# Kernel tuning notes

Hardware: AMD Instinct MI355X
Metric: run time of the kernel (lower is better)

## Reference

```python
import jax, jax.numpy as jnp
import numpy as np

IMG = 448; P = 16; C = 3; D = 512; DC = 8; DS = 4
NH = IMG // P            # 28 patches per side
NPATCH = NH * NH         # 784
PDIM = C * P * P         # 768
BATCH = 32
EPS = 1e-5


def setup_inputs() -> dict:
    key = jax.random.key(0)
    ks = jax.random.split(key, 10)
    def lin(k, fan_in, shape):
        bound = 1.0 / np.sqrt(fan_in)
        return jax.random.uniform(k, shape, jnp.float32, -bound, bound)
    return {
        "images": jax.random.normal(ks[0], (BATCH, C, IMG, IMG), jnp.float32),
        "W_patch": lin(ks[1], PDIM, (PDIM, D)),
        "b_patch": jnp.zeros((D,), jnp.float32),
        "pos_embed": jax.random.normal(ks[2], (1, NPATCH, D), jnp.float32) * 0.02,
        "W_coord": lin(ks[3], D, (D, DC)),
        "b_coord": jnp.zeros((DC,), jnp.float32),
        "W_spinor": lin(ks[4], D, (D, DS)),
        "b_spinor": jnp.zeros((DS,), jnp.float32),
        "W_embed": lin(ks[5], DC, (DC, D)),
        "b_embed": jnp.zeros((D,), jnp.float32),
        "ln_gamma": jnp.ones((D,), jnp.float32),
        "ln_beta": jnp.zeros((D,), jnp.float32),
        "W_out": lin(ks[6], D, (D, D)),
        "b_out": jnp.zeros((D,), jnp.float32),
    }


def reference(images, W_patch, b_patch, pos_embed, W_coord, b_coord,
              W_spinor, b_spinor, W_embed, b_embed,
              ln_gamma, ln_beta, W_out, b_out):
    B = images.shape[0]
    # patchify == F.unfold(kernel=stride=P).transpose(1,2):
    # patches[b, bh*NH+bw, c*P*P + i*P + j] = images[b, c, bh*P+i, bw*P+j]
    patches = images.reshape(B, C, NH, P, NH, P)
    patches = patches.transpose(0, 2, 4, 1, 3, 5).reshape(B, NPATCH, PDIM)
    # patch embed + positional embedding  -> (B, NPATCH, D)
    x = patches @ W_patch + b_patch + pos_embed
    # manifold projection: coords (B,N,DC), spinor (B,N,DS)
    coords = x @ W_coord + b_coord
    spinor = x @ W_spinor + b_spinor
    # K0 scalar bilinear: psi^T psi -> (B, N)
    K0 = jnp.sum(spinor * spinor, axis=-1)
    # embed back from manifold coords -> (B, N, D)
    x_manifold = coords @ W_embed + b_embed
    # K0-modulated remix + residual
    x_enh = x_manifold * K0[..., None] + x
    # output projection: LayerNorm -> Linear
    mu = jnp.mean(x_enh, axis=-1, keepdims=True)
    var = jnp.mean(jnp.square(x_enh - mu), axis=-1, keepdims=True)
    x_norm = (x_enh - mu) * jax.lax.rsqrt(var + EPS) * ln_gamma + ln_beta
    return x_norm @ W_out + b_out
```

## Files before the change

kernel.cpp:

```cpp
#include <hip/hip_runtime.h>
#include <hip/hip_bf16.h>
#include <stdint.h>


typedef __bf16 bf16_t;
typedef bf16_t bf16x8 __attribute__((ext_vector_type(8)));
typedef bf16_t bf16x4 __attribute__((ext_vector_type(4)));
typedef float  f32x4  __attribute__((ext_vector_type(4)));

#define IMG     448
#define PSZ     16
#define NHP     28
#define NPATCH  784
#define PDIM    768
#define DMODEL  512
#define MROWS   25088

__device__ __forceinline__ void gload16(void* lds, const void* g) {
  __builtin_amdgcn_global_load_lds(
      (__attribute__((address_space(1))) void*)(uintptr_t)g,
      (__attribute__((address_space(3))) void*)lds,
      16, 0, 0);
}

__device__ __forceinline__ unsigned short bfbits(float v) {
  bf16_t h = (bf16_t)v;
  unsigned short u;
  __builtin_memcpy(&u, &h, 2);
  return u;
}
__device__ __forceinline__ float f_from_bits(unsigned u) {
  float f; __builtin_memcpy(&f, &u, 4); return f;
}

__global__ __launch_bounds__(256) void transpose_to_bf16(
    const float* __restrict__ src, bf16_t* __restrict__ dst, int K, int N)
{
  __shared__ float t[64][65];
  const int tx = threadIdx.x;
  const int ty = threadIdx.y;
  const int bx = blockIdx.x * 64;
  const int by = blockIdx.y * 64;
  #pragma unroll
  for (int r = ty; r < 64; r += 4)
    t[r][tx] = src[(size_t)(by + r) * N + (bx + tx)];
  __syncthreads();
  #pragma unroll
  for (int r = ty; r < 64; r += 4)
    dst[(size_t)(bx + r) * K + (by + tx)] = (bf16_t)t[tx][r];
}

__global__ __launch_bounds__(256) void manifold_prep(
    const float* __restrict__ Wc, const float* __restrict__ Ws,
    const float* __restrict__ We, const float* __restrict__ be,
    bf16_t* __restrict__ Wcsg, bf16_t* __restrict__ We2g)
{
  const int idx = blockIdx.x * 256 + threadIdx.x;
  if (idx < 8192) {
    const int r = idx >> 9, n = idx & 511;
    float v = 0.f;
    if (r < 8)       v = Wc[n * 8 + r];
    else if (r < 12) v = Ws[n * 4 + (r - 8)];
    Wcsg[idx] = (bf16_t)v;
  } else {
    const int j = idx - 8192;
    const int n = j >> 4, k = j & 15;
    float v = 0.f;
    if (k < 8)       v = We[k * 512 + n];
    else if (k == 8) v = be[n];
    We2g[j] = (bf16_t)v;
  }
}

__global__ __launch_bounds__(256) void patchify_bf16(
    const float* __restrict__ images, bf16_t* __restrict__ Apat)
{
  __shared__ bf16_t t[16][456];
  const int tid = threadIdx.x;
  const int bid = blockIdx.x;
  const int b = bid / 84, rem = bid % 84;
  const int c = rem / 28, ph = rem % 28;
  const float* src = images + ((size_t)(b * 3 + c) * IMG + ph * PSZ) * IMG;

  #pragma unroll
  for (int idx = tid; idx < 16 * 112; idx += 256) {
    const int i = idx / 112, x4 = idx % 112;
    const float4 v = *(const float4*)(src + (size_t)i * IMG + x4 * 4);
    bf16x4 w;
    w[0] = (bf16_t)v.x; w[1] = (bf16_t)v.y; w[2] = (bf16_t)v.z; w[3] = (bf16_t)v.w;
    *(bf16x4*)&t[i][x4 * 4] = w;
  }
  __syncthreads();

  const size_t mbase = (size_t)b * NPATCH + (size_t)ph * NHP;
  #pragma unroll
  for (int idx = tid; idx < 28 * 64; idx += 256) {
    const int pw = idx >> 6, e = idx & 63;
    const int i = e >> 2, j4 = e & 3;
    const bf16x4 w = *(const bf16x4*)&t[i][pw * 16 + j4 * 4];
    *(bf16x4*)&Apat[(mbase + pw) * PDIM + c * 256 + i * 16 + j4 * 4] = w;
  }
}

template<int KDIM, int EPI>
__global__ __launch_bounds__(256) void gemm_bf16(
    const bf16_t* __restrict__ A, const bf16_t* __restrict__ BT,
    const float* __restrict__ bias, const float* __restrict__ pos,
    void* __restrict__ outp)
{
  __shared__ bf16_t As[64 * 64];
  __shared__ bf16_t Bs[128 * 64];
  constexpr int NT = KDIM / 64;

  const int tid  = threadIdx.x;
  const int orig = blockIdx.x;
  const int wg   = (orig & 7) * 196 + (orig >> 3);
  const int n0   = (wg & 3) * 128;
  const int m0   = (wg >> 2) * 64;

  const int wave = tid >> 6, lane = tid & 63;

  const int ra = lane >> 3;
  const int ca = (lane & 7) ^ ra;
  const bf16_t* ag = A  + (size_t)(m0 + wave * 8 + ra) * KDIM + ca * 8;
  const bf16_t* bg = BT + (size_t)(n0 + wave * 8 + ra) * KDIM + ca * 8;
  bf16_t* al0 = As + (wave * 8) * 64;
  bf16_t* al1 = As + (wave * 8 + 32) * 64;
  bf16_t* bl0 = Bs + (wave * 8) * 64;
  bf16_t* bl1 = Bs + (wave * 8 + 32) * 64;
  bf16_t* bl2 = Bs + (wave * 8 + 64) * 64;
  bf16_t* bl3 = Bs + (wave * 8 + 96) * 64;

  const int wm = (wave >> 1) * 32;
  const int wn = (wave & 1) * 64;
  const int lr = lane & 15;
  const int lt = lane >> 4;

  f32x4 acc[2][4] = {};

  for (int t = 0; t < NT; ++t) {
    const int k0 = t * 64;
    __syncthreads();
    gload16(al0, ag + k0);
    gload16(al1, ag + 32 * KDIM + k0);
    gload16(bl0, bg + k0);
    gload16(bl1, bg + 32 * KDIM + k0);
    gload16(bl2, bg + 64 * KDIM + k0);
    gload16(bl3, bg + 96 * KDIM + k0);
    __syncthreads();

    #pragma unroll
    for (int ks = 0; ks < 2; ++ks) {
      const int c = ks * 4 + lt;
      bf16x8 af[2], bfr[4];
      #pragma unroll
      for (int i = 0; i < 2; ++i) {
        const int row = wm + i * 16 + lr;
        af[i] = *(const bf16x8*)&As[row * 64 + ((c ^ (row & 7)) * 8)];
      }
      #pragma unroll
      for (int j = 0; j < 4; ++j) {
        const int row = wn + j * 16 + lr;
        bfr[j] = *(const bf16x8*)&Bs[row * 64 + ((c ^ (row & 7)) * 8)];
      }
      #pragma unroll
      for (int i = 0; i < 2; ++i)
        #pragma unroll
        for (int j = 0; j < 4; ++j)
          acc[i][j] = __builtin_amdgcn_mfma_f32_16x16x32_bf16(af[i], bfr[j], acc[i][j], 0, 0, 0);
    }
  }

  const int q4 = lt << 2;
  const int colb = n0 + wn;
  #pragma unroll
  for (int i = 0; i < 2; ++i) {
    #pragma unroll
    for (int r = 0; r < 4; ++r) {
      const int mm = m0 + wm + i * 16 + q4 + r;
      if (EPI == 0) {
        const int pp = mm % NPATCH;
        const float* pe = pos + (size_t)pp * DMODEL;
        bf16_t* orow = (bf16_t*)outp + (size_t)mm * DMODEL;
        #pragma unroll
        for (int j = 0; j < 4; ++j) {
          const int nn = colb + j * 16 + lr;
          orow[nn] = (bf16_t)(acc[i][j][r] + bias[nn] + pe[nn]);
        }
      } else {
        float* orow = (float*)outp + (size_t)mm * DMODEL;
        #pragma unroll
        for (int j = 0; j < 4; ++j) {
          const int nn = colb + j * 16 + lr;
          orow[nn] = acc[i][j][r] + bias[nn];
        }
      }
    }
  }
}

__global__ __launch_bounds__(256) void gemm1_fused_fallback(
    const float* __restrict__ images, const bf16_t* __restrict__ WpT,
    const float* __restrict__ b_patch, const float* __restrict__ pos_embed,
    bf16_t* __restrict__ xout)
{
  __shared__ bf16_t As[128][40];
  __shared__ bf16_t Bs[128][40];
  const int tid = threadIdx.x;
  const int n0 = blockIdx.x * 128;
  const int m0 = blockIdx.y * 128;
  const int sr = tid >> 1;
  const int sh = tid & 1;
  const int m  = m0 + sr;
  const int b  = m / NPATCH;
  const int p  = m - b * NPATCH;
  const int ph = p / NHP;
  const int pw = p - ph * NHP;
  const float* abase = images + (size_t)(b * 3) * (IMG * IMG)
                              + (size_t)(ph * PSZ) * IMG + pw * PSZ;
  const bf16_t* brow = WpT + (size_t)(n0 + sr) * PDIM + sh * 16;
  const int wave = tid >> 6;
  const int lane = tid & 63;
  const int wm = (wave >> 1) << 6;
  const int wn = (wave & 1) << 6;
  const int lr = lane & 15;
  const int lk = (lane >> 4) << 3;
  f32x4 acc[4][4] = {};
  for (int ks = 0; ks < PDIM / 32; ++ks) {
    const int k0 = ks * 32;
    const int c  = k0 >> 8;
    const int ib = (k0 >> 4) & 15;
    const float* asrc = abase + (size_t)c * (IMG * IMG) + (ib + sh) * IMG;
    const float4 av0 = *(const float4*)(asrc + 0);
    const float4 av1 = *(const float4*)(asrc + 4);
    const float4 av2 = *(const float4*)(asrc + 8);
    const float4 av3 = *(const float4*)(asrc + 12);
    const uint4 bv0 = *(const uint4*)(brow + k0);
    const uint4 bv1 = *(const uint4*)(brow + k0 + 8);
    __syncthreads();
    bf16x8 a0, a1;
    a0[0] = (bf16_t)av0.x; a0[1] = (bf16_t)av0.y; a0[2] = (bf16_t)av0.z; a0[3] = (bf16_t)av0.w;
    a0[4] = (bf16_t)av1.x; a0[5] = (bf16_t)av1.y; a0[6] = (bf16_t)av1.z; a0[7] = (bf16_t)av1.w;
    a1[0] = (bf16_t)av2.x; a1[1] = (bf16_t)av2.y; a1[2] = (bf16_t)av2.z; a1[3] = (bf16_t)av2.w;
    a1[4] = (bf16_t)av3.x; a1[5] = (bf16_t)av3.y; a1[6] = (bf16_t)av3.z; a1[7] = (bf16_t)av3.w;
    *(bf16x8*)&As[sr][sh * 16]     = a0;
    *(bf16x8*)&As[sr][sh * 16 + 8] = a1;
    *(uint4*)&Bs[sr][sh * 16]      = bv0;
    *(uint4*)&Bs[sr][sh * 16 + 8]  = bv1;
    __syncthreads();
    bf16x8 af[4], bfr[4];
    #pragma unroll
    for (int i = 0; i < 4; ++i) af[i]  = *(const bf16x8*)&As[wm + i * 16 + lr][lk];
    #pragma unroll
    for (int j = 0; j < 4; ++j) bfr[j] = *(const bf16x8*)&Bs[wn + j * 16 + lr][lk];
    #pragma unroll
    for (int i = 0; i < 4; ++i)
      #pragma unroll
      for (int j = 0; j < 4; ++j)
        acc[i][j] = __builtin_amdgcn_mfma_f32_16x16x32_bf16(af[i], bfr[j], acc[i][j], 0, 0, 0);
  }
  const int colb = n0 + wn;
  #pragma unroll
  for (int i = 0; i < 4; ++i) {
    #pragma unroll
    for (int r = 0; r < 4; ++r) {
      const int mm = m0 + wm + i * 16 + ((lane >> 4) << 2) + r;
      const int pp = mm % NPATCH;
      const float* pe = pos_embed + (size_t)pp * DMODEL;
      bf16_t* orow = xout + (size_t)mm * DMODEL;
      #pragma unroll
      for (int j = 0; j < 4; ++j) {
        const int nn = colb + j * 16 + lr;
        orow[nn] = (bf16_t)(acc[i][j][r] + b_patch[nn] + pe[nn]);
      }
    }
  }
}

__global__ __launch_bounds__(256) void manifold_ln_v4(
    bf16_t* __restrict__ x,
    const bf16_t* __restrict__ Wcsg, const bf16_t* __restrict__ We2g,
    const float* __restrict__ b_coord, const float* __restrict__ b_spinor,
    const float* __restrict__ ln_gamma, const float* __restrict__ ln_beta)
{
  __shared__ bf16_t sWcs[16 * 512];
  __shared__ bf16_t sWe2[512 * 16];
  __shared__ float  sg[512], sb[512];

  const int tid = threadIdx.x;

  #pragma unroll
  for (int i = 0; i < 4; ++i) {
    const int c = tid + 256 * i;
    const int r = c >> 6, off = (c & 63) * 16;
    const uint4 v = *(const uint4*)((const char*)Wcsg + (size_t)c * 16);
    *(uint4*)((char*)sWcs + ((r * 1024 + off) ^ ((r & 7) << 4))) = v;
  }
  #pragma unroll
  for (int i = 0; i < 4; ++i) {
    const int c = tid + 256 * i;
    const int n = c >> 1, half = (c & 1) * 16;
    const uint4 v = *(const uint4*)((const char*)We2g + (size_t)c * 16);
    *(uint4*)((char*)sWe2 + ((n * 32 + half) ^ ((n & 3) << 4))) = v;
  }
  for (int i = tid; i < 512; i += 256) {
    sg[i] = ln_gamma[i];
    sb[i] = ln_beta[i];
  }
  __syncthreads();

  const int w    = tid >> 6;
  const int lane = tid & 63;
  const int lr   = lane & 15;
  const int lk   = (lane >> 4) << 3;
  const int q4   = (lane >> 4) << 2;
  const int m0w  = blockIdx.x * 64 + w * 16;

  float bbv[4];
  #pragma unroll
  for (int r = 0; r < 4; ++r) {
    if (q4 == 0)      bbv[r] = b_coord[r];
    else if (q4 == 4) bbv[r] = b_coord[4 + r];
    else if (q4 == 8) bbv[r] = b_spinor[r];
    else              bbv[r] = 0.f;
  }

  const bf16_t* xrow = x + (size_t)(m0w + lr) * DMODEL + lk;
  f32x4 acc1 = {0.f, 0.f, 0.f, 0.f};
  #pragma unroll
  for (int ks = 0; ks < 16; ++ks) {
    const bf16x8 bf = *(const bf16x8*)(xrow + ks * 32);
    const int wb = (lr * 1024 + ks * 64 + lk * 2) ^ ((lr & 7) << 4);
    const bf16x8 wf = *(const bf16x8*)((const char*)sWcs + wb);
    acc1 = __builtin_amdgcn_mfma_f32_16x16x32_bf16(wf, bf, acc1, 0, 0, 0);
  }

  float sv[4];
  #pragma unroll
  for (int r = 0; r < 4; ++r) sv[r] = acc1[r] + bbv[r];

  const float k0own = sv[0] * sv[0] + sv[1] * sv[1] + sv[2] * sv[2] + sv[3] * sv[3];
  const float k0v = __shfl(k0own, 32 + lr, 64);

  float ov[4];
  #pragma unroll
  for (int r = 0; r < 4; ++r) ov[r] = __shfl_xor(sv[r], 16, 64);

  const bf16_t zb = (bf16_t)0.f;
  bf16x8 b2;
  if (lk == 0) {
    #pragma unroll
    for (int r = 0; r < 4; ++r) { b2[r] = (bf16_t)sv[r]; b2[4 + r] = (bf16_t)ov[r]; }
  } else if (lk == 8) {
    b2[0] = (bf16_t)1.0f;
    #pragma unroll
    for (int t = 1; t < 8; ++t) b2[t] = zb;
  } else {
    #pragma unroll
    for (int t = 0; t < 8; ++t) b2[t] = zb;
  }

  const bf16_t* xres = x + (size_t)(m0w + lr) * DMODEL + q4;
  unsigned xpA[32], xpB[32];
  float s1 = 0.f, s2 = 0.f;
  #pragma unroll
  for (int nf = 0; nf < 32; ++nf) {
    const int n = nf * 16 + lr;
    const int wb = (n * 32 + lk * 2) ^ ((n & 3) << 4);
    const bf16x8 wf = *(const bf16x8*)((const char*)sWe2 + wb);
    f32x4 acc2 = {0.f, 0.f, 0.f, 0.f};
    acc2 = __builtin_amdgcn_mfma_f32_16x16x32_bf16(wf, b2, acc2, 0, 0, 0);

    const bf16x4 xr = *(const bf16x4*)(xres + nf * 16);
    float xe[4];
    #pragma unroll
    for (int r = 0; r < 4; ++r) {
      xe[r] = acc2[r] * k0v + (float)xr[r];
      s1 += xe[r];
      s2 += xe[r] * xe[r];
    }
    xpA[nf] = (unsigned)bfbits(xe[0]) | ((unsigned)bfbits(xe[1]) << 16);
    xpB[nf] = (unsigned)bfbits(xe[2]) | ((unsigned)bfbits(xe[3]) << 16);
  }

  s1 += __shfl_xor(s1, 16, 64);
  s1 += __shfl_xor(s1, 32, 64);
  s2 += __shfl_xor(s2, 16, 64);
  s2 += __shfl_xor(s2, 32, 64);
  const float mu  = s1 * (1.f / 512.f);
  const float var = s2 * (1.f / 512.f) - mu * mu;
  const float rsg = rsqrtf(var + 1e-5f);

  bf16_t* xo = x + (size_t)(m0w + lr) * DMODEL + q4;
  #pragma unroll
  for (int nf = 0; nf < 32; ++nf) {
    const f32x4 g = *(const f32x4*)&sg[nf * 16 + q4];
    const f32x4 b = *(const f32x4*)&sb[nf * 16 + q4];
    const float v0 = f_from_bits(xpA[nf] << 16);
    const float v1 = f_from_bits(xpA[nf] & 0xffff0000u);
    const float v2 = f_from_bits(xpB[nf] << 16);
    const float v3 = f_from_bits(xpB[nf] & 0xffff0000u);
    bf16x4 o;
    o[0] = (bf16_t)((v0 - mu) * rsg * g[0] + b[0]);
    o[1] = (bf16_t)((v1 - mu) * rsg * g[1] + b[1]);
    o[2] = (bf16_t)((v2 - mu) * rsg * g[2] + b[2]);
    o[3] = (bf16_t)((v3 - mu) * rsg * g[3] + b[3]);
    *(bf16x4*)(xo + nf * 16) = o;
  }
}

extern "C" void kernel_launch(void* const* d_in, const int* in_sizes, int n_in,
                              void* d_out, int out_size, void* d_ws, size_t ws_size,
                              hipStream_t stream)
{
  const float* images    = (const float*)d_in[0];
  const float* W_patch   = (const float*)d_in[1];
  const float* b_patch   = (const float*)d_in[2];
  const float* pos_embed = (const float*)d_in[3];
  const float* W_coord   = (const float*)d_in[4];
  const float* b_coord   = (const float*)d_in[5];
  const float* W_spinor  = (const float*)d_in[6];
  const float* b_spinor  = (const float*)d_in[7];
  const float* W_embed   = (const float*)d_in[8];
  const float* b_embed   = (const float*)d_in[9];
  const float* ln_gamma  = (const float*)d_in[10];
  const float* ln_beta   = (const float*)d_in[11];
  const float* W_out     = (const float*)d_in[12];
  const float* b_out     = (const float*)d_in[13];
  float* out = (float*)d_out;

  const size_t SZ_APAT = (size_t)MROWS * PDIM * 2;
  const size_t SZ_X    = (size_t)MROWS * DMODEL * 2;
  const size_t SZ_WPT  = (size_t)DMODEL * PDIM * 2;
  const size_t SZ_WOT  = (size_t)DMODEL * DMODEL * 2;
  const size_t SZ_WCS  = 16 * 512 * 2;
  const size_t SZ_WE2  = 512 * 16 * 2;
  const size_t NEED_FULL = SZ_APAT + SZ_X + SZ_WPT + SZ_WOT + SZ_WCS + SZ_WE2;

  char* ws = (char*)d_ws;
  const bool full = (ws_size >= NEED_FULL);

  bf16_t *Apat, *x, *WpT, *WoT, *Wcsg, *We2g;
  if (full) {
    char* p = ws;
    Apat  = (bf16_t*)p;            p += SZ_APAT;
    x     = (bf16_t*)p;            p += SZ_X;
    WpT   = (bf16_t*)p;            p += SZ_WPT;
    WoT   = (bf16_t*)p;            p += SZ_WOT;
    Wcsg  = (bf16_t*)p;            p += SZ_WCS;
    We2g  = (bf16_t*)p;
  } else {
    char* p = ws;
    Apat  = nullptr;
    x     = (bf16_t*)p;            p += SZ_X;
    WpT   = (bf16_t*)p;            p += SZ_WPT;
    WoT   = (bf16_t*)p;            p += SZ_WOT;
    Wcsg  = (bf16_t*)p;            p += SZ_WCS;
    We2g  = (bf16_t*)p;
  }

  hipLaunchKernelGGL(transpose_to_bf16, dim3(8, 12), dim3(64, 4), 0, stream,
                     W_patch, WpT, PDIM, DMODEL);
  hipLaunchKernelGGL(transpose_to_bf16, dim3(8, 8), dim3(64, 4), 0, stream,
                     W_out, WoT, DMODEL, DMODEL);
  hipLaunchKernelGGL(manifold_prep, dim3(64), dim3(256), 0, stream,
                     W_coord, W_spinor, W_embed, b_embed, Wcsg, We2g);

  if (full) {
    hipLaunchKernelGGL(patchify_bf16, dim3(32 * 3 * 28), dim3(256), 0, stream,
                       images, Apat);
    hipLaunchKernelGGL((gemm_bf16<PDIM, 0>), dim3(1568), dim3(256), 0, stream,
                       Apat, WpT, b_patch, pos_embed, (void*)x);
  } else {
    hipLaunchKernelGGL(gemm1_fused_fallback, dim3(4, 196), dim3(256), 0, stream,
                       images, WpT, b_patch, pos_embed, x);
  }

  hipLaunchKernelGGL(manifold_ln_v4, dim3(392), dim3(256), 0, stream,
                     x, Wcsg, We2g, b_coord, b_spinor, ln_gamma, ln_beta);

  hipLaunchKernelGGL((gemm_bf16<DMODEL, 1>), dim3(1568), dim3(256), 0, stream,
                     x, WoT, b_out, (const float*)nullptr, (void*)out);
}
```

Before: 114.5 us.

## Split manifold+LayerNorm into coords/K0 kernel and row-wise embed+LN kernel

Replaces the single fused manifold_ln kernel with two kernels. coords_k0 computes the coords and K0 per row with an MFMA and stores them in a small fp32 buffer. embed_ln then rebuilds x_manifold with scalar FMAs from register-resident W_embed and applies LayerNorm, one row per wave with fully coalesced 16-byte accesses. The intent is to drop the LDS staging, the second tiny MFMA and the 64 packed registers per thread, for better occupancy and memory access. In exchange x is read twice plus one extra launch and a small buffer round trip, and x_manifold and b_embed now stay in fp32 instead of bf16.

```diff
diff --git a/kernel.cpp b/kernel.cpp
--- a/kernel.cpp
+++ b/kernel.cpp
@@ -23,16 +23,6 @@
       16, 0, 0);
 }
 
-__device__ __forceinline__ unsigned short bfbits(float v) {
-  bf16_t h = (bf16_t)v;
-  unsigned short u;
-  __builtin_memcpy(&u, &h, 2);
-  return u;
-}
-__device__ __forceinline__ float f_from_bits(unsigned u) {
-  float f; __builtin_memcpy(&f, &u, 4); return f;
-}
-
 __global__ __launch_bounds__(256) void transpose_to_bf16(
     const float* __restrict__ src, bf16_t* __restrict__ dst, int K, int N)
 {
@@ -52,8 +42,7 @@
 
 __global__ __launch_bounds__(256) void manifold_prep(
     const float* __restrict__ Wc, const float* __restrict__ Ws,
-    const float* __restrict__ We, const float* __restrict__ be,
-    bf16_t* __restrict__ Wcsg, bf16_t* __restrict__ We2g)
+    bf16_t* __restrict__ Wcsg)
 {
   const int idx = blockIdx.x * 256 + threadIdx.x;
   if (idx < 8192) {
@@ -62,13 +51,6 @@
     if (r < 8)       v = Wc[n * 8 + r];
     else if (r < 12) v = Ws[n * 4 + (r - 8)];
     Wcsg[idx] = (bf16_t)v;
-  } else {
-    const int j = idx - 8192;
-    const int n = j >> 4, k = j & 15;
-    float v = 0.f;
-    if (k < 8)       v = We[k * 512 + n];
-    else if (k == 8) v = be[n];
-    We2g[j] = (bf16_t)v;
   }
 }
 
@@ -277,44 +259,16 @@
   }
 }
 
-__global__ __launch_bounds__(256) void manifold_ln_v4(
-    bf16_t* __restrict__ x,
-    const bf16_t* __restrict__ Wcsg, const bf16_t* __restrict__ We2g,
+__global__ __launch_bounds__(64) void coords_k0(
+    const bf16_t* __restrict__ x, const bf16_t* __restrict__ Wcsg,
     const float* __restrict__ b_coord, const float* __restrict__ b_spinor,
-    const float* __restrict__ ln_gamma, const float* __restrict__ ln_beta)
-{
-  __shared__ bf16_t sWcs[16 * 512];
-  __shared__ bf16_t sWe2[512 * 16];
-  __shared__ float  sg[512], sb[512];
-
-  const int tid = threadIdx.x;
-
-  #pragma unroll
-  for (int i = 0; i < 4; ++i) {
-    const int c = tid + 256 * i;
-    const int r = c >> 6, off = (c & 63) * 16;
-    const uint4 v = *(const uint4*)((const char*)Wcsg + (size_t)c * 16);
-    *(uint4*)((char*)sWcs + ((r * 1024 + off) ^ ((r & 7) << 4))) = v;
-  }
-  #pragma unroll
-  for (int i = 0; i < 4; ++i) {
-    const int c = tid + 256 * i;
-    const int n = c >> 1, half = (c & 1) * 16;
-    const uint4 v = *(const uint4*)((const char*)We2g + (size_t)c * 16);
-    *(uint4*)((char*)sWe2 + ((n * 32 + half) ^ ((n & 3) << 4))) = v;
-  }
-  for (int i = tid; i < 512; i += 256) {
-    sg[i] = ln_gamma[i];
-    sb[i] = ln_beta[i];
-  }
-  __syncthreads();
-
-  const int w    = tid >> 6;
-  const int lane = tid & 63;
+    float* __restrict__ Cbuf)
+{
+  const int lane = threadIdx.x;
   const int lr   = lane & 15;
   const int lk   = (lane >> 4) << 3;
   const int q4   = (lane >> 4) << 2;
-  const int m0w  = blockIdx.x * 64 + w * 16;
+  const int m0w  = blockIdx.x * 16;
 
   float bbv[4];
   #pragma unroll
@@ -326,12 +280,12 @@
   }
 
   const bf16_t* xrow = x + (size_t)(m0w + lr) * DMODEL + lk;
+  const bf16_t* wrow = Wcsg + lr * DMODEL + lk;
   f32x4 acc1 = {0.f, 0.f, 0.f, 0.f};
   #pragma unroll
   for (int ks = 0; ks < 16; ++ks) {
     const bf16x8 bf = *(const bf16x8*)(xrow + ks * 32);
-    const int wb = (lr * 1024 + ks * 64 + lk * 2) ^ ((lr & 7) << 4);
-    const bf16x8 wf = *(const bf16x8*)((const char*)sWcs + wb);
+    const bf16x8 wf = *(const bf16x8*)(wrow + ks * 32);
     acc1 = __builtin_amdgcn_mfma_f32_16x16x32_bf16(wf, bf, acc1, 0, 0, 0);
   }
 
@@ -339,73 +293,86 @@
   #pragma unroll
   for (int r = 0; r < 4; ++r) sv[r] = acc1[r] + bbv[r];
 
-  const float k0own = sv[0] * sv[0] + sv[1] * sv[1] + sv[2] * sv[2] + sv[3] * sv[3];
-  const float k0v = __shfl(k0own, 32 + lr, 64);
-
-  float ov[4];
-  #pragma unroll
-  for (int r = 0; r < 4; ++r) ov[r] = __shfl_xor(sv[r], 16, 64);
-
-  const bf16_t zb = (bf16_t)0.f;
-  bf16x8 b2;
-  if (lk == 0) {
-    #pragma unroll
-    for (int r = 0; r < 4; ++r) { b2[r] = (bf16_t)sv[r]; b2[4 + r] = (bf16_t)ov[r]; }
-  } else if (lk == 8) {
-    b2[0] = (bf16_t)1.0f;
-    #pragma unroll
-    for (int t = 1; t < 8; ++t) b2[t] = zb;
-  } else {
-    #pragma unroll
-    for (int t = 0; t < 8; ++t) b2[t] = zb;
-  }
-
-  const bf16_t* xres = x + (size_t)(m0w + lr) * DMODEL + q4;
-  unsigned xpA[32], xpB[32];
-  float s1 = 0.f, s2 = 0.f;
-  #pragma unroll
-  for (int nf = 0; nf < 32; ++nf) {
-    const int n = nf * 16 + lr;
-    const int wb = (n * 32 + lk * 2) ^ ((n & 3) << 4);
-    const bf16x8 wf = *(const bf16x8*)((const char*)sWe2 + wb);
-    f32x4 acc2 = {0.f, 0.f, 0.f, 0.f};
-    acc2 = __builtin_amdgcn_mfma_f32_16x16x32_bf16(wf, b2, acc2, 0, 0, 0);
-
-    const bf16x4 xr = *(const bf16x4*)(xres + nf * 16);
-    float xe[4];
-    #pragma unroll
-    for (int r = 0; r < 4; ++r) {
-      xe[r] = acc2[r] * k0v + (float)xr[r];
-      s1 += xe[r];
-      s2 += xe[r] * xe[r];
-    }
-    xpA[nf] = (unsigned)bfbits(xe[0]) | ((unsigned)bfbits(xe[1]) << 16);
-    xpB[nf] = (unsigned)bfbits(xe[2]) | ((unsigned)bfbits(xe[3]) << 16);
-  }
-
-  s1 += __shfl_xor(s1, 16, 64);
-  s1 += __shfl_xor(s1, 32, 64);
-  s2 += __shfl_xor(s2, 16, 64);
-  s2 += __shfl_xor(s2, 32, 64);
-  const float mu  = s1 * (1.f / 512.f);
-  const float var = s2 * (1.f / 512.f) - mu * mu;
-  const float rsg = rsqrtf(var + 1e-5f);
-
-  bf16_t* xo = x + (size_t)(m0w + lr) * DMODEL + q4;
-  #pragma unroll
-  for (int nf = 0; nf < 32; ++nf) {
-    const f32x4 g = *(const f32x4*)&sg[nf * 16 + q4];
-    const f32x4 b = *(const f32x4*)&sb[nf * 16 + q4];
-    const float v0 = f_from_bits(xpA[nf] << 16);
-    const float v1 = f_from_bits(xpA[nf] & 0xffff0000u);
-    const float v2 = f_from_bits(xpB[nf] << 16);
-    const float v3 = f_from_bits(xpB[nf] & 0xffff0000u);
-    bf16x4 o;
-    o[0] = (bf16_t)((v0 - mu) * rsg * g[0] + b[0]);
-    o[1] = (bf16_t)((v1 - mu) * rsg * g[1] + b[1]);
-    o[2] = (bf16_t)((v2 - mu) * rsg * g[2] + b[2]);
-    o[3] = (bf16_t)((v3 - mu) * rsg * g[3] + b[3]);
-    *(bf16x4*)(xo + nf * 16) = o;
+  float* crow = Cbuf + (size_t)(m0w + lr) * 12;
+  if (q4 == 8) {
+    crow[8] = sv[0] * sv[0] + sv[1] * sv[1] + sv[2] * sv[2] + sv[3] * sv[3];
+  } else if (q4 == 0 || q4 == 4) {
+    f32x4 st = {sv[0], sv[1], sv[2], sv[3]};
+    *(f32x4*)(crow + q4) = st;
+  }
+}
+
+__global__ __launch_bounds__(256) void embed_ln(
+    bf16_t* __restrict__ x, const float* __restrict__ Cbuf,
+    const float* __restrict__ We, const float* __restrict__ be,
+    const float* __restrict__ gamma, const float* __restrict__ beta)
+{
+  const int w    = threadIdx.x >> 6;
+  const int lane = threadIdx.x & 63;
+  const int n0   = lane * 8;
+
+  f32x4 wlo[8], whi[8];
+  #pragma unroll
+  for (int dc = 0; dc < 8; ++dc) {
+    wlo[dc] = *(const f32x4*)&We[dc * DMODEL + n0];
+    whi[dc] = *(const f32x4*)&We[dc * DMODEL + n0 + 4];
+  }
+  const f32x4 beL = *(const f32x4*)&be[n0];
+  const f32x4 beH = *(const f32x4*)&be[n0 + 4];
+  const f32x4 gL  = *(const f32x4*)&gamma[n0];
+  const f32x4 gH  = *(const f32x4*)&gamma[n0 + 4];
+  const f32x4 btL = *(const f32x4*)&beta[n0];
+  const f32x4 btH = *(const f32x4*)&beta[n0 + 4];
+
+  const size_t base = (size_t)blockIdx.x * 32 + w * 8;
+  #pragma unroll 2
+  for (int rr = 0; rr < 8; ++rr) {
+    const size_t row = base + rr;
+    const bf16x8 xv = *(const bf16x8*)(x + row * DMODEL + n0);
+    const float* crow = Cbuf + row * 12;
+    const f32x4 c0 = *(const f32x4*)(crow);
+    const f32x4 c1 = *(const f32x4*)(crow + 4);
+    const float k0 = crow[8];
+
+    float v[8];
+    float s1 = 0.f, s2 = 0.f;
+    #pragma unroll
+    for (int e = 0; e < 4; ++e) {
+      float xm = beL[e];
+      #pragma unroll
+      for (int dc = 0; dc < 4; ++dc) xm += c0[dc] * wlo[dc][e];
+      #pragma unroll
+      for (int dc = 0; dc < 4; ++dc) xm += c1[dc] * wlo[4 + dc][e];
+      const float vv = xm * k0 + (float)xv[e];
+      v[e] = vv; s1 += vv; s2 += vv * vv;
+    }
+    #pragma unroll
+    for (int e = 0; e < 4; ++e) {
+      float xm = beH[e];
+      #pragma unroll
+      for (int dc = 0; dc < 4; ++dc) xm += c0[dc] * whi[dc][e];
+      #pragma unroll
+      for (int dc = 0; dc < 4; ++dc) xm += c1[dc] * whi[4 + dc][e];
+      const float vv = xm * k0 + (float)xv[4 + e];
+      v[4 + e] = vv; s1 += vv; s2 += vv * vv;
+    }
+
+    #pragma unroll
+    for (int off = 1; off <= 32; off <<= 1) {
+      s1 += __shfl_xor(s1, off, 64);
+      s2 += __shfl_xor(s2, off, 64);
+    }
+    const float mu  = s1 * (1.f / 512.f);
+    const float var = s2 * (1.f / 512.f) - mu * mu;
+    const float rs  = rsqrtf(var + 1e-5f);
+
+    bf16x8 o;
+    #pragma unroll
+    for (int e = 0; e < 4; ++e) {
+      o[e]     = (bf16_t)((v[e]     - mu) * rs * gL[e] + btL[e]);
+      o[4 + e] = (bf16_t)((v[4 + e] - mu) * rs * gH[e] + btH[e]);
+    }
+    *(bf16x8*)(x + row * DMODEL + n0) = o;
   }
 }
 
@@ -434,13 +401,14 @@
   const size_t SZ_WPT  = (size_t)DMODEL * PDIM * 2;
   const size_t SZ_WOT  = (size_t)DMODEL * DMODEL * 2;
   const size_t SZ_WCS  = 16 * 512 * 2;
-  const size_t SZ_WE2  = 512 * 16 * 2;
-  const size_t NEED_FULL = SZ_APAT + SZ_X + SZ_WPT + SZ_WOT + SZ_WCS + SZ_WE2;
+  const size_t SZ_CBUF = (size_t)MROWS * 12 * 4;
+  const size_t NEED_FULL = SZ_APAT + SZ_X + SZ_WPT + SZ_WOT + SZ_WCS + SZ_CBUF;
 
   char* ws = (char*)d_ws;
   const bool full = (ws_size >= NEED_FULL);
 
-  bf16_t *Apat, *x, *WpT, *WoT, *Wcsg, *We2g;
+  bf16_t *Apat, *x, *WpT, *WoT, *Wcsg;
+  float *Cbuf;
   if (full) {
     char* p = ws;
     Apat  = (bf16_t*)p;            p += SZ_APAT;
@@ -448,7 +416,7 @@
     WpT   = (bf16_t*)p;            p += SZ_WPT;
     WoT   = (bf16_t*)p;            p += SZ_WOT;
     Wcsg  = (bf16_t*)p;            p += SZ_WCS;
-    We2g  = (bf16_t*)p;
+    Cbuf  = (float*)p;
   } else {
     char* p = ws;
     Apat  = nullptr;
@@ -456,15 +424,15 @@
     WpT   = (bf16_t*)p;            p += SZ_WPT;
     WoT   = (bf16_t*)p;            p += SZ_WOT;
     Wcsg  = (bf16_t*)p;            p += SZ_WCS;
-    We2g  = (bf16_t*)p;
+    Cbuf  = (float*)p;
   }
 
   hipLaunchKernelGGL(transpose_to_bf16, dim3(8, 12), dim3(64, 4), 0, stream,
                      W_patch, WpT, PDIM, DMODEL);
   hipLaunchKernelGGL(transpose_to_bf16, dim3(8, 8), dim3(64, 4), 0, stream,
                      W_out, WoT, DMODEL, DMODEL);
-  hipLaunchKernelGGL(manifold_prep, dim3(64), dim3(256), 0, stream,
-                     W_coord, W_spinor, W_embed, b_embed, Wcsg, We2g);
+  hipLaunchKernelGGL(manifold_prep, dim3(32), dim3(256), 0, stream,
+                     W_coord, W_spinor, Wcsg);
 
   if (full) {
     hipLaunchKernelGGL(patchify_bf16, dim3(32 * 3 * 28), dim3(256), 0, stream,
@@ -476,8 +444,10 @@
                        images, WpT, b_patch, pos_embed, x);
   }
 
-  hipLaunchKernelGGL(manifold_ln_v4, dim3(392), dim3(256), 0, stream,
-                     x, Wcsg, We2g, b_coord, b_spinor, ln_gamma, ln_beta);
+  hipLaunchKernelGGL(coords_k0, dim3(MROWS / 16), dim3(64), 0, stream,
+                     x, Wcsg, b_coord, b_spinor, Cbuf);
+  hipLaunchKernelGGL(embed_ln, dim3(MROWS / 32), dim3(256), 0, stream,
+                     x, Cbuf, W_embed, b_embed, ln_gamma, ln_beta);
 
   hipLaunchKernelGGL((gemm_bf16<DMODEL, 1>), dim3(1568), dim3(256), 0, stream,
                      x, WoT, b_out, (const float*)nullptr, (void*)out);
```

Result: no change. 112.6 us (-1.7%).
